# Performance work log

Measured on AMD Instinct MI355X. Metric: run time of the kernel, lower is better.

## Reference

```python
import jax, jax.numpy as jnp
import numpy as np

N = 8192
E = 262144
H = 8
D_IN = 256
D_OUT = 256
D_PRIME = D_OUT // H  # is_concat=True


def setup_inputs() -> dict:
    key = jax.random.key(0)
    k_x, k_e, k_ww, k_wb, k_aw, k_ab = jax.random.split(key, 6)
    scale_w = 1.0 / np.sqrt(D_IN)
    scale_a = 1.0 / np.sqrt(2 * D_PRIME)
    return {
        "x": jax.random.normal(k_x, (N, D_IN), dtype=jnp.float32),
        "edge_index": jax.random.randint(k_e, (2, E), 0, N, dtype=jnp.int64),
        "W_w": jax.random.uniform(k_ww, (H, D_PRIME, D_IN), jnp.float32, -scale_w, scale_w),
        "W_b": jax.random.uniform(k_wb, (H, D_PRIME), jnp.float32, -scale_w, scale_w),
        "a_w": jax.random.uniform(k_aw, (H, 1, 2 * D_PRIME), jnp.float32, -scale_a, scale_a),
        "a_b": jax.random.uniform(k_ab, (H, 1), jnp.float32, -scale_a, scale_a),
    }


def reference(x, edge_index, W_w, W_b, a_w, a_b):
    n = x.shape[0]
    vi, vj = edge_index[0], edge_index[1]
    heads = []
    for k in range(W_w.shape[0]):  # small fixed head loop
        Wx = x @ W_w[k].T + W_b[k]                       # [N, d']
        pair = jnp.concatenate([Wx[vi], Wx[vj]], axis=-1)  # [E, 2d']
        e = jax.nn.leaky_relu(pair @ a_w[k].T + a_b[k], negative_slope=0.2)[:, 0]  # [E]
        # dense NxN score matrix: non-edges keep score 0 and DO participate in softmax,
        # duplicate edges accumulate -- matches torch scatter_add_ + Softmax(dim=-1)
        A = jnp.zeros((n, n), dtype=x.dtype).at[vi, vj].add(e)
        heads.append(jax.nn.softmax(A, axis=-1) @ Wx)     # [N, d']
    xp = jnp.stack(heads)                                 # [H, N, d']
    xp = jnp.transpose(xp, (1, 0, 2)).reshape(n, -1)      # is_concat=True
    return jax.nn.elu(xp)
```

## Files before the change

kernel.cpp:

```cpp
#include <hip/hip_runtime.h>
#include <hip/hip_fp16.h>


constexpr int N_NODES = 8192;
constexpr int E_EDGES = 262144;
constexpr int DIN = 256;
constexpr int DOUT = 256;
constexpr int MAXROW = 96;
constexpr unsigned POISON = 0xAAAAAAAAu;

constexpr int BUCKET_BLOCKS = E_EDGES / (256 * 4);
constexpr int GEMM_BLOCKS = (N_NODES / 128) * 8;

typedef __attribute__((ext_vector_type(8))) short bf16x8;
typedef __attribute__((ext_vector_type(4))) float f32x4;

__device__ __forceinline__ float leaky02(float v) { return v > 0.f ? v : 0.2f * v; }

__device__ __forceinline__ float4 ldh4(const __half* p) {
    int2 r = *(const int2*)p;
    __half2 a = *(__half2*)&r.x;
    __half2 b = *(__half2*)&r.y;
    float2 fa = __half22float2(a);
    float2 fb = __half22float2(b);
    return make_float4(fa.x, fa.y, fb.x, fb.y);
}

__device__ __forceinline__ void split4(const float4 v, int2& hi, int2& lo) {
    unsigned u0 = __float_as_uint(v.x), u1 = __float_as_uint(v.y);
    unsigned u2 = __float_as_uint(v.z), u3 = __float_as_uint(v.w);
    unsigned h0 = u0 & 0xffff0000u, h1 = u1 & 0xffff0000u;
    unsigned h2 = u2 & 0xffff0000u, h3 = u3 & 0xffff0000u;
    hi.x = (int)((u0 >> 16) | h1);
    hi.y = (int)((u2 >> 16) | h3);
    float l0 = v.x - __uint_as_float(h0);
    float l1 = v.y - __uint_as_float(h1);
    float l2 = v.z - __uint_as_float(h2);
    float l3 = v.w - __uint_as_float(h3);
    lo.x = (int)((__float_as_uint(l0) >> 16) | (__float_as_uint(l1) & 0xffff0000u));
    lo.y = (int)((__float_as_uint(l2) >> 16) | (__float_as_uint(l3) & 0xffff0000u));
}

__global__ __launch_bounds__(256) void gemm_bucket(
    const float* __restrict__ x, const float* __restrict__ W,
    const float* __restrict__ Wb, const float* __restrict__ a_w,
    const int* __restrict__ eidx,
    __half* __restrict__ Wx, float* __restrict__ asrc_t,
    float* __restrict__ adst_t, float* __restrict__ colsum,
    unsigned* __restrict__ counts, int* __restrict__ colbuf)
{
    __shared__ short Whi[32][264], Wlo[32][264];
    __shared__ short Ahi[2][128][40], Alo[2][128][40];
    const int t = threadIdx.x;

    if (blockIdx.x < BUCKET_BLOCKS) {
        const int e0 = blockIdx.x * 1024 + t * 4;
        const int4 vi4 = *(const int4*)&eidx[e0];
        const int4 vj4 = *(const int4*)&eidx[E_EDGES + e0];
        unsigned c;
        c = atomicAdd(&counts[vi4.x], 1u) - POISON; if (c < MAXROW) colbuf[(size_t)vi4.x * MAXROW + c] = vj4.x;
        c = atomicAdd(&counts[vi4.y], 1u) - POISON; if (c < MAXROW) colbuf[(size_t)vi4.y * MAXROW + c] = vj4.y;
        c = atomicAdd(&counts[vi4.z], 1u) - POISON; if (c < MAXROW) colbuf[(size_t)vi4.z * MAXROW + c] = vj4.z;
        c = atomicAdd(&counts[vi4.w], 1u) - POISON; if (c < MAXROW) colbuf[(size_t)vi4.w * MAXROW + c] = vj4.w;
        return;
    }

    const int gb = blockIdx.x - BUCKET_BLOCKS;
    const int bm = gb >> 3;
    const int h  = gb & 7;
    const int r0 = bm * 128;
    const int w = t >> 6;
    const int lane = t & 63;
    const int lanen = lane & 15, quad = lane >> 4;

    float4 wl[8], al[4];
#pragma unroll
    for (int j = 0; j < 8; ++j) {
        const int idx = j * 256 + t;
        const int n = idx >> 6, q = idx & 63;
        wl[j] = *(const float4*)&W[((size_t)(h * 32 + n)) * DIN + q * 4];
    }
#pragma unroll
    for (int j = 0; j < 4; ++j) {
        const int idx = j * 256 + t;
        const int row = idx >> 3, q = idx & 7;
        al[j] = *(const float4*)&x[(size_t)(r0 + row) * DIN + q * 4];
    }
#pragma unroll
    for (int j = 0; j < 8; ++j) {
        const int idx = j * 256 + t;
        const int n = idx >> 6, q = idx & 63;
        int2 hi, lo;
        split4(wl[j], hi, lo);
        *(int2*)&Whi[n][q * 4] = hi;
        *(int2*)&Wlo[n][q * 4] = lo;
    }
#pragma unroll
    for (int j = 0; j < 4; ++j) {
        const int idx = j * 256 + t;
        const int row = idx >> 3, q = idx & 7;
        int2 hi, lo;
        split4(al[j], hi, lo);
        *(int2*)&Ahi[0][row][q * 4] = hi;
        *(int2*)&Alo[0][row][q * 4] = lo;
    }

    f32x4 acc[2][2] = {};

    for (int c = 0; c < 8; ++c) {
        __syncthreads();
        float4 nv[4];
        if (c < 7) {
#pragma unroll
            for (int j = 0; j < 4; ++j) {
                const int idx = j * 256 + t;
                const int row = idx >> 3, q = idx & 7;
                nv[j] = *(const float4*)&x[(size_t)(r0 + row) * DIN + (c + 1) * 32 + q * 4];
            }
        }
        const int buf = c & 1;
        bf16x8 bh0 = *(const bf16x8*)&Whi[lanen][c * 32 + quad * 8];
        bf16x8 bl0 = *(const bf16x8*)&Wlo[lanen][c * 32 + quad * 8];
        bf16x8 bh1 = *(const bf16x8*)&Whi[16 + lanen][c * 32 + quad * 8];
        bf16x8 bl1 = *(const bf16x8*)&Wlo[16 + lanen][c * 32 + quad * 8];
#pragma unroll
        for (int ms = 0; ms < 2; ++ms) {
            const int arow = w * 32 + ms * 16 + lanen;
            bf16x8 ah = *(const bf16x8*)&Ahi[buf][arow][quad * 8];
            bf16x8 al2 = *(const bf16x8*)&Alo[buf][arow][quad * 8];
            acc[ms][0] = __builtin_amdgcn_mfma_f32_16x16x32_bf16(ah, bh0, acc[ms][0], 0, 0, 0);
            acc[ms][0] = __builtin_amdgcn_mfma_f32_16x16x32_bf16(ah, bl0, acc[ms][0], 0, 0, 0);
            acc[ms][0] = __builtin_amdgcn_mfma_f32_16x16x32_bf16(al2, bh0, acc[ms][0], 0, 0, 0);
            acc[ms][1] = __builtin_amdgcn_mfma_f32_16x16x32_bf16(ah, bh1, acc[ms][1], 0, 0, 0);
            acc[ms][1] = __builtin_amdgcn_mfma_f32_16x16x32_bf16(ah, bl1, acc[ms][1], 0, 0, 0);
            acc[ms][1] = __builtin_amdgcn_mfma_f32_16x16x32_bf16(al2, bh1, acc[ms][1], 0, 0, 0);
        }
        if (c < 7) {
            const int nbuf = (c + 1) & 1;
#pragma unroll
            for (int j = 0; j < 4; ++j) {
                const int idx = j * 256 + t;
                const int row = idx >> 3, q = idx & 7;
                int2 hi, lo;
                split4(nv[j], hi, lo);
                *(int2*)&Ahi[nbuf][row][q * 4] = hi;
                *(int2*)&Alo[nbuf][row][q * 4] = lo;
            }
        }
    }

    const float bias0 = Wb[h * 32 + lanen];
    const float bias1 = Wb[h * 32 + 16 + lanen];
    const float aws0 = a_w[h * 64 + lanen];
    const float aws1 = a_w[h * 64 + 16 + lanen];
    const float awd0 = a_w[h * 64 + 32 + lanen];
    const float awd1 = a_w[h * 64 + 48 + lanen];
    float cs0 = 0.f, cs1 = 0.f;

#pragma unroll
    for (int ms = 0; ms < 2; ++ms) {
        const int rowb = r0 + w * 32 + ms * 16 + quad * 4;
        float ps[4], pd[4];
#pragma unroll
        for (int r = 0; r < 4; ++r) {
            const float a0 = acc[ms][0][r] + bias0;
            const float a1 = acc[ms][1][r] + bias1;
            Wx[(size_t)(rowb + r) * DOUT + h * 32 + lanen] = __float2half_rn(a0);
            Wx[(size_t)(rowb + r) * DOUT + h * 32 + 16 + lanen] = __float2half_rn(a1);
            ps[r] = a0 * aws0 + a1 * aws1;
            pd[r] = a0 * awd0 + a1 * awd1;
            cs0 += a0;
            cs1 += a1;
        }
#pragma unroll
        for (int msk = 1; msk <= 8; msk <<= 1)
#pragma unroll
            for (int r = 0; r < 4; ++r) {
                ps[r] += __shfl_xor(ps[r], msk);
                pd[r] += __shfl_xor(pd[r], msk);
            }
        if (lanen == 0) {
#pragma unroll
            for (int r = 0; r < 4; ++r) {
                asrc_t[(size_t)(rowb + r) * 8 + h] = ps[r];
                adst_t[(size_t)(rowb + r) * 8 + h] = pd[r];
            }
        }
    }
#pragma unroll
    for (int msk = 16; msk <= 32; msk <<= 1) {
        cs0 += __shfl_xor(cs0, msk);
        cs1 += __shfl_xor(cs1, msk);
    }
    if (lane < 16) {
        atomicAdd(&colsum[h * 32 + lanen], cs0);
        atomicAdd(&colsum[h * 32 + 16 + lanen], cs1);
    }
}

__global__ __launch_bounds__(256) void row_softmax(
    const unsigned* __restrict__ counts, const int* __restrict__ colbuf,
    const __half* __restrict__ Wx, const float* __restrict__ asrc_t,
    const float* __restrict__ adst_t, const float* __restrict__ a_b,
    const float* __restrict__ colsum, float* __restrict__ out)
{
    const int w = threadIdx.x >> 6;
    const int lane = threadIdx.x & 63;
    const int i = blockIdx.x * 4 + w;

    __shared__ alignas(16) int   colsL[4][MAXROW];
    __shared__ alignas(16) float wv[4][MAXROW][8];
    __shared__ alignas(16) float sv[4][MAXROW];
    __shared__ alignas(16) float base_s[4][8];

    int len = (int)(counts[i] - POISON);
    if ((unsigned)len > MAXROW) len = MAXROW;

    for (int p = lane; p < len; p += 64) colsL[w][p] = colbuf[(size_t)i * MAXROW + p];
    __builtin_amdgcn_wave_barrier();

    if (len <= 64) {
        const bool act = lane < len;
        const int c = act ? colsL[w][lane] : 0;
        const int c_cmp = act ? c : (0x40000000 + lane);
        bool dupb = false;
        for (int k = 1; k < 64; ++k) {
            int cq = __shfl(c_cmp, (lane - k) & 63);
            dupb = dupb || ((k <= lane) && (cq == c_cmp));
        }
        const bool isrep = act && !dupb;
        const int nd = __popcll(__ballot(isrep));
        const bool anydup = (nd != len);
        const float fnd = (float)(N_NODES - nd);

#pragma unroll
        for (int ck = 0; ck < 2; ++ck) {
            const float4 as = *(const float4*)&asrc_t[(size_t)i * 8 + ck * 4];
            const float4 ab = *(const float4*)&a_b[ck * 4];
            const float4 ad = *(const float4*)&adst_t[(size_t)c * 8 + ck * 4];
            float s[4], sm[4];
            s[0] = leaky02(as.x + ab.x + ad.x);
            s[1] = leaky02(as.y + ab.y + ad.y);
            s[2] = leaky02(as.z + ab.z + ad.z);
            s[3] = leaky02(as.w + ab.w + ad.w);
#pragma unroll
            for (int hh = 0; hh < 4; ++hh) sm[hh] = s[hh];

            if (anydup) {
                for (int k = 1; k < 64; ++k) {
                    const int sl = (lane + k) & 63;
                    const int cq = __shfl(c_cmp, sl);
                    float sq[4];
#pragma unroll
                    for (int hh = 0; hh < 4; ++hh) sq[hh] = __shfl(s[hh], sl);
                    if (cq == c_cmp) {
#pragma unroll
                        for (int hh = 0; hh < 4; ++hh) sm[hh] += sq[hh];
                    }
                }
            }

            float val[4];
#pragma unroll
            for (int hh = 0; hh < 4; ++hh) val[hh] = isrep ? sm[hh] : 0.f;
#pragma unroll
            for (int st = 32; st; st >>= 1)
#pragma unroll
                for (int hh = 0; hh < 4; ++hh) val[hh] = fmaxf(val[hh], __shfl_xor(val[hh], st));
            float enm[4], e[4];
#pragma unroll
            for (int hh = 0; hh < 4; ++hh) {
                float m = fmaxf(val[hh], 0.f);
                enm[hh] = __expf(-m);
                e[hh] = isrep ? __expf(sm[hh] - m) : 0.f;
                val[hh] = e[hh];
            }
#pragma unroll
            for (int st = 32; st; st >>= 1)
#pragma unroll
                for (int hh = 0; hh < 4; ++hh) val[hh] += __shfl_xor(val[hh], st);
            float wt[4];
#pragma unroll
            for (int hh = 0; hh < 4; ++hh) {
                float invZ = 1.f / (val[hh] + fnd * enm[hh]);
                wt[hh] = isrep ? (e[hh] - enm[hh]) * invZ : 0.f;
                enm[hh] *= invZ;
            }
            if (act) {
                float4 wq; wq.x = wt[0]; wq.y = wt[1]; wq.z = wt[2]; wq.w = wt[3];
                *(float4*)&wv[w][lane][ck * 4] = wq;
            }
            if (lane == 0) {
                float4 bq; bq.x = enm[0]; bq.y = enm[1]; bq.z = enm[2]; bq.w = enm[3];
                *(float4*)&base_s[w][ck * 4] = bq;
            }
        }
    } else {
        int repf0 = 0, repf1 = 0;
        {
            int p = lane;
            if (p < len) {
                int cc = colsL[w][p]; int r = 1;
                for (int q = 0; q < p; ++q) if (colsL[w][q] == cc) { r = 0; break; }
                repf0 = r;
            }
            p = lane + 64;
            if (p < len) {
                int cc = colsL[w][p]; int r = 1;
                for (int q = 0; q < p; ++q) if (colsL[w][q] == cc) { r = 0; break; }
                repf1 = r;
            }
        }
        int ndloc = repf0 + repf1;
#pragma unroll
        for (int st = 32; st; st >>= 1) ndloc += __shfl_xor(ndloc, st);
        const int nd = ndloc;
        for (int hh = 0; hh < 8; ++hh) {
            const float sabh = asrc_t[(size_t)i * 8 + hh] + a_b[hh];
            for (int p = lane; p < len; p += 64)
                sv[w][p] = leaky02(sabh + adst_t[(size_t)colsL[w][p] * 8 + hh]);
            __builtin_amdgcn_wave_barrier();
            float lmax = -1e30f, sm0 = 0.f, sm1 = 0.f;
            if (lane < len && repf0) {
                int cc = colsL[w][lane]; float a = sv[w][lane];
                for (int q = lane + 1; q < len; ++q) if (colsL[w][q] == cc) a += sv[w][q];
                sm0 = a; lmax = fmaxf(lmax, a);
            }
            if (lane + 64 < len && repf1) {
                int cc = colsL[w][lane + 64]; float a = sv[w][lane + 64];
                for (int q = lane + 65; q < len; ++q) if (colsL[w][q] == cc) a += sv[w][q];
                sm1 = a; lmax = fmaxf(lmax, a);
            }
#pragma unroll
            for (int st = 32; st; st >>= 1) lmax = fmaxf(lmax, __shfl_xor(lmax, st));
            const float mh = fmaxf(lmax, 0.f), enm = __expf(-mh);
            float e0 = (lane < len && repf0) ? __expf(sm0 - mh) : 0.f;
            float e1 = (lane + 64 < len && repf1) ? __expf(sm1 - mh) : 0.f;
            float lsum = e0 + e1;
#pragma unroll
            for (int st = 32; st; st >>= 1) lsum += __shfl_xor(lsum, st);
            const float Z = lsum + (float)(N_NODES - nd) * enm, invZ = 1.f / Z;
            if (lane == 0) base_s[w][hh] = enm * invZ;
            if (lane < len)      wv[w][lane][hh]      = repf0 ? (e0 - enm) * invZ : 0.f;
            if (lane + 64 < len) wv[w][lane + 64][hh] = repf1 ? (e1 - enm) * invZ : 0.f;
            __builtin_amdgcn_wave_barrier();
        }
    }

    const int len8 = (len + 7) & ~7;
    for (int p = len + lane; p < len8; p += 64) {
        colsL[w][p] = 0;
        float4 z; z.x = 0.f; z.y = 0.f; z.z = 0.f; z.w = 0.f;
        *(float4*)&wv[w][p][0] = z;
        *(float4*)&wv[w][p][4] = z;
    }
    __builtin_amdgcn_wave_barrier();

    const int h4 = lane >> 3;
    const float bsel = base_s[w][h4];
    const int col4 = lane * 4;

    float4 acc0; acc0.x = 0.f; acc0.y = 0.f; acc0.z = 0.f; acc0.w = 0.f;
    float4 acc1 = acc0;
    for (int p0 = 0; p0 < len8; p0 += 8) {
        const int4 ca = *(const int4*)&colsL[w][p0];
        const int4 cb = *(const int4*)&colsL[w][p0 + 4];
        const float4 v0 = ldh4(&Wx[(size_t)ca.x * DOUT + col4]);
        const float4 v1 = ldh4(&Wx[(size_t)ca.y * DOUT + col4]);
        const float4 v2 = ldh4(&Wx[(size_t)ca.z * DOUT + col4]);
        const float4 v3 = ldh4(&Wx[(size_t)ca.w * DOUT + col4]);
        const float4 v4 = ldh4(&Wx[(size_t)cb.x * DOUT + col4]);
        const float4 v5 = ldh4(&Wx[(size_t)cb.y * DOUT + col4]);
        const float4 v6 = ldh4(&Wx[(size_t)cb.z * DOUT + col4]);
        const float4 v7 = ldh4(&Wx[(size_t)cb.w * DOUT + col4]);
        const float w0 = wv[w][p0 + 0][h4];
        const float w1 = wv[w][p0 + 1][h4];
        const float w2 = wv[w][p0 + 2][h4];
        const float w3 = wv[w][p0 + 3][h4];
        const float w4 = wv[w][p0 + 4][h4];
        const float w5 = wv[w][p0 + 5][h4];
        const float w6 = wv[w][p0 + 6][h4];
        const float w7 = wv[w][p0 + 7][h4];
        acc0.x = fmaf(w0, v0.x, acc0.x); acc0.y = fmaf(w0, v0.y, acc0.y);
        acc0.z = fmaf(w0, v0.z, acc0.z); acc0.w = fmaf(w0, v0.w, acc0.w);
        acc1.x = fmaf(w1, v1.x, acc1.x); acc1.y = fmaf(w1, v1.y, acc1.y);
        acc1.z = fmaf(w1, v1.z, acc1.z); acc1.w = fmaf(w1, v1.w, acc1.w);
        acc0.x = fmaf(w2, v2.x, acc0.x); acc0.y = fmaf(w2, v2.y, acc0.y);
        acc0.z = fmaf(w2, v2.z, acc0.z); acc0.w = fmaf(w2, v2.w, acc0.w);
        acc1.x = fmaf(w3, v3.x, acc1.x); acc1.y = fmaf(w3, v3.y, acc1.y);
        acc1.z = fmaf(w3, v3.z, acc1.z); acc1.w = fmaf(w3, v3.w, acc1.w);
        acc0.x = fmaf(w4, v4.x, acc0.x); acc0.y = fmaf(w4, v4.y, acc0.y);
        acc0.z = fmaf(w4, v4.z, acc0.z); acc0.w = fmaf(w4, v4.w, acc0.w);
        acc1.x = fmaf(w5, v5.x, acc1.x); acc1.y = fmaf(w5, v5.y, acc1.y);
        acc1.z = fmaf(w5, v5.z, acc1.z); acc1.w = fmaf(w5, v5.w, acc1.w);
        acc0.x = fmaf(w6, v6.x, acc0.x); acc0.y = fmaf(w6, v6.y, acc0.y);
        acc0.z = fmaf(w6, v6.z, acc0.z); acc0.w = fmaf(w6, v6.w, acc0.w);
        acc1.x = fmaf(w7, v7.x, acc1.x); acc1.y = fmaf(w7, v7.y, acc1.y);
        acc1.z = fmaf(w7, v7.z, acc1.z); acc1.w = fmaf(w7, v7.w, acc1.w);
    }
    const float4 cs = *(const float4*)&colsum[col4];
    float4 o;
    o.x = fmaf(bsel, cs.x, acc0.x + acc1.x);
    o.y = fmaf(bsel, cs.y, acc0.y + acc1.y);
    o.z = fmaf(bsel, cs.z, acc0.z + acc1.z);
    o.w = fmaf(bsel, cs.w, acc0.w + acc1.w);
    o.x = o.x > 0.f ? o.x : expm1f(o.x);
    o.y = o.y > 0.f ? o.y : expm1f(o.y);
    o.z = o.z > 0.f ? o.z : expm1f(o.z);
    o.w = o.w > 0.f ? o.w : expm1f(o.w);
    *(float4*)&out[(size_t)i * DOUT + col4] = o;
}

extern "C" void kernel_launch(void* const* d_in, const int* in_sizes, int n_in,
                              void* d_out, int out_size, void* d_ws, size_t ws_size,
                              hipStream_t stream) {
    const float* x   = (const float*)d_in[0];
    const int*   ei  = (const int*)d_in[1];
    const float* W_w = (const float*)d_in[2];
    const float* W_b = (const float*)d_in[3];
    const float* a_w = (const float*)d_in[4];
    const float* a_b = (const float*)d_in[5];
    float* out = (float*)d_out;

    char* ws = (char*)d_ws;
    size_t off = 0;
    __half* Wx = (__half*)(ws + off);      off += (size_t)N_NODES * DOUT * 2;
    float* colsum = (float*)(ws + off);    off += DOUT * 4;
    unsigned* counts = (unsigned*)(ws + off); off += (size_t)N_NODES * 4;
    int* colbuf = (int*)(ws + off);        off += (size_t)N_NODES * MAXROW * 4;
    float* asrc_t = (float*)(ws + off);    off += (size_t)N_NODES * 8 * 4;
    float* adst_t = (float*)(ws + off);    off += (size_t)N_NODES * 8 * 4;
    (void)ws_size; (void)in_sizes; (void)n_in; (void)out_size;

    gemm_bucket<<<BUCKET_BLOCKS + GEMM_BLOCKS, 256, 0, stream>>>(
        x, W_w, W_b, a_w, ei, Wx, asrc_t, adst_t, colsum, counts, colbuf);
    row_softmax<<<N_NODES / 4, 256, 0, stream>>>(counts, colbuf, Wx, asrc_t,
                                                 adst_t, a_b, colsum, out);
}
```

Before: 132.1 us.

## Fuse GEMM, bucketing and row softmax into one cooperative grid-synced kernel

Merges the two kernels into a single cooperative launch of 512 blocks. Each block first buckets its share of edges, then computes one GEMM tile, then waits at a grid-wide sync before handling 16 rows of the softmax-aggregate phase. Shared memory is reused between the phases through a union. The aim is to drop the second launch and the gap between kernels. In exchange the grid is capped at 512 blocks, which lowers parallelism in the softmax phase, and the grid sync adds its own cost. The fused kernel also has to fit co-residency limits for the cooperative launch.

```diff
diff --git a/kernel.cpp b/kernel.cpp
--- a/kernel.cpp
+++ b/kernel.cpp
@@ -1,5 +1,8 @@
 #include <hip/hip_runtime.h>
 #include <hip/hip_fp16.h>
+#include <hip/hip_cooperative_groups.h>
+
+namespace cg = cooperative_groups;
 
 
 constexpr int N_NODES = 8192;
@@ -9,8 +12,8 @@
 constexpr int MAXROW = 96;
 constexpr unsigned POISON = 0xAAAAAAAAu;
 
-constexpr int BUCKET_BLOCKS = E_EDGES / (256 * 4);
-constexpr int GEMM_BLOCKS = (N_NODES / 128) * 8;
+constexpr int NBLK = 512;
+constexpr int EDGES_PER_BLK = E_EDGES / NBLK;
 
 typedef __attribute__((ext_vector_type(8))) short bf16x8;
 typedef __attribute__((ext_vector_type(4))) float f32x4;
@@ -41,374 +44,377 @@
     lo.y = (int)((__float_as_uint(l2) >> 16) | (__float_as_uint(l3) & 0xffff0000u));
 }
 
-__global__ __launch_bounds__(256) void gemm_bucket(
+__global__ __launch_bounds__(256) void gat_fused(
     const float* __restrict__ x, const float* __restrict__ W,
     const float* __restrict__ Wb, const float* __restrict__ a_w,
-    const int* __restrict__ eidx,
+    const int* __restrict__ eidx, const float* __restrict__ a_b,
     __half* __restrict__ Wx, float* __restrict__ asrc_t,
     float* __restrict__ adst_t, float* __restrict__ colsum,
-    unsigned* __restrict__ counts, int* __restrict__ colbuf)
+    unsigned* __restrict__ counts, int* __restrict__ colbuf,
+    float* __restrict__ out)
 {
-    __shared__ short Whi[32][264], Wlo[32][264];
-    __shared__ short Ahi[2][128][40], Alo[2][128][40];
+    __shared__ union {
+        struct {
+            short Whi[32][264], Wlo[32][264];
+            short Ahi[2][128][40], Alo[2][128][40];
+        } g;
+        struct {
+            int   colsL[4][MAXROW];
+            float wv[4][MAXROW][8];
+            float sv[4][MAXROW];
+            float base_s[4][8];
+        } s;
+    } smem;
+
     const int t = threadIdx.x;
-
-    if (blockIdx.x < BUCKET_BLOCKS) {
-        const int e0 = blockIdx.x * 1024 + t * 4;
-        const int4 vi4 = *(const int4*)&eidx[e0];
-        const int4 vj4 = *(const int4*)&eidx[E_EDGES + e0];
-        unsigned c;
-        c = atomicAdd(&counts[vi4.x], 1u) - POISON; if (c < MAXROW) colbuf[(size_t)vi4.x * MAXROW + c] = vj4.x;
-        c = atomicAdd(&counts[vi4.y], 1u) - POISON; if (c < MAXROW) colbuf[(size_t)vi4.y * MAXROW + c] = vj4.y;
-        c = atomicAdd(&counts[vi4.z], 1u) - POISON; if (c < MAXROW) colbuf[(size_t)vi4.z * MAXROW + c] = vj4.z;
-        c = atomicAdd(&counts[vi4.w], 1u) - POISON; if (c < MAXROW) colbuf[(size_t)vi4.w * MAXROW + c] = vj4.w;
-        return;
-    }
-
-    const int gb = blockIdx.x - BUCKET_BLOCKS;
-    const int bm = gb >> 3;
-    const int h  = gb & 7;
-    const int r0 = bm * 128;
     const int w = t >> 6;
     const int lane = t & 63;
-    const int lanen = lane & 15, quad = lane >> 4;
-
-    float4 wl[8], al[4];
-#pragma unroll
-    for (int j = 0; j < 8; ++j) {
-        const int idx = j * 256 + t;
-        const int n = idx >> 6, q = idx & 63;
-        wl[j] = *(const float4*)&W[((size_t)(h * 32 + n)) * DIN + q * 4];
+
+    {
+        const int e0 = blockIdx.x * EDGES_PER_BLK + t * 2;
+        const int2 vi2 = *(const int2*)&eidx[e0];
+        const int2 vj2 = *(const int2*)&eidx[E_EDGES + e0];
+        unsigned c;
+        c = atomicAdd(&counts[vi2.x], 1u) - POISON; if (c < MAXROW) colbuf[(size_t)vi2.x * MAXROW + c] = vj2.x;
+        c = atomicAdd(&counts[vi2.y], 1u) - POISON; if (c < MAXROW) colbuf[(size_t)vi2.y * MAXROW + c] = vj2.y;
     }
-#pragma unroll
-    for (int j = 0; j < 4; ++j) {
-        const int idx = j * 256 + t;
-        const int row = idx >> 3, q = idx & 7;
-        al[j] = *(const float4*)&x[(size_t)(r0 + row) * DIN + q * 4];
+
+    {
+        const int gb = blockIdx.x;
+        const int bm = gb >> 3;
+        const int h  = gb & 7;
+        const int r0 = bm * 128;
+        const int lanen = lane & 15, quad = lane >> 4;
+
+        float4 wl[8], al[4];
+#pragma unroll
+        for (int j = 0; j < 8; ++j) {
+            const int idx = j * 256 + t;
+            const int n = idx >> 6, q = idx & 63;
+            wl[j] = *(const float4*)&W[((size_t)(h * 32 + n)) * DIN + q * 4];
+        }
+#pragma unroll
+        for (int j = 0; j < 4; ++j) {
+            const int idx = j * 256 + t;
+            const int row = idx >> 3, q = idx & 7;
+            al[j] = *(const float4*)&x[(size_t)(r0 + row) * DIN + q * 4];
+        }
+#pragma unroll
+        for (int j = 0; j < 8; ++j) {
+            const int idx = j * 256 + t;
+            const int n = idx >> 6, q = idx & 63;
+            int2 hi, lo;
+            split4(wl[j], hi, lo);
+            *(int2*)&smem.g.Whi[n][q * 4] = hi;
+            *(int2*)&smem.g.Wlo[n][q * 4] = lo;
+        }
+#pragma unroll
+        for (int j = 0; j < 4; ++j) {
+            const int idx = j * 256 + t;
+            const int row = idx >> 3, q = idx & 7;
+            int2 hi, lo;
+            split4(al[j], hi, lo);
+            *(int2*)&smem.g.Ahi[0][row][q * 4] = hi;
+            *(int2*)&smem.g.Alo[0][row][q * 4] = lo;
+        }
+
+        f32x4 acc[2][2] = {};
+
+        for (int c = 0; c < 8; ++c) {
+            __syncthreads();
+            float4 nv[4];
+            if (c < 7) {
+#pragma unroll
+                for (int j = 0; j < 4; ++j) {
+                    const int idx = j * 256 + t;
+                    const int row = idx >> 3, q = idx & 7;
+                    nv[j] = *(const float4*)&x[(size_t)(r0 + row) * DIN + (c + 1) * 32 + q * 4];
+                }
+            }
+            const int buf = c & 1;
+            bf16x8 bh0 = *(const bf16x8*)&smem.g.Whi[lanen][c * 32 + quad * 8];
+            bf16x8 bl0 = *(const bf16x8*)&smem.g.Wlo[lanen][c * 32 + quad * 8];
+            bf16x8 bh1 = *(const bf16x8*)&smem.g.Whi[16 + lanen][c * 32 + quad * 8];
+            bf16x8 bl1 = *(const bf16x8*)&smem.g.Wlo[16 + lanen][c * 32 + quad * 8];
+#pragma unroll
+            for (int ms = 0; ms < 2; ++ms) {
+                const int arow = w * 32 + ms * 16 + lanen;
+                bf16x8 ah = *(const bf16x8*)&smem.g.Ahi[buf][arow][quad * 8];
+                bf16x8 al2 = *(const bf16x8*)&smem.g.Alo[buf][arow][quad * 8];
+                acc[ms][0] = __builtin_amdgcn_mfma_f32_16x16x32_bf16(ah, bh0, acc[ms][0], 0, 0, 0);
+                acc[ms][0] = __builtin_amdgcn_mfma_f32_16x16x32_bf16(ah, bl0, acc[ms][0], 0, 0, 0);
+                acc[ms][0] = __builtin_amdgcn_mfma_f32_16x16x32_bf16(al2, bh0, acc[ms][0], 0, 0, 0);
+                acc[ms][1] = __builtin_amdgcn_mfma_f32_16x16x32_bf16(ah, bh1, acc[ms][1], 0, 0, 0);
+                acc[ms][1] = __builtin_amdgcn_mfma_f32_16x16x32_bf16(ah, bl1, acc[ms][1], 0, 0, 0);
+                acc[ms][1] = __builtin_amdgcn_mfma_f32_16x16x32_bf16(al2, bh1, acc[ms][1], 0, 0, 0);
+            }
+            if (c < 7) {
+                const int nbuf = (c + 1) & 1;
+#pragma unroll
+                for (int j = 0; j < 4; ++j) {
+                    const int idx = j * 256 + t;
+                    const int row = idx >> 3, q = idx & 7;
+                    int2 hi, lo;
+                    split4(nv[j], hi, lo);
+                    *(int2*)&smem.g.Ahi[nbuf][row][q * 4] = hi;
+                    *(int2*)&smem.g.Alo[nbuf][row][q * 4] = lo;
+                }
+            }
+        }
+
+        const float bias0 = Wb[h * 32 + lanen];
+        const float bias1 = Wb[h * 32 + 16 + lanen];
+        const float aws0 = a_w[h * 64 + lanen];
+        const float aws1 = a_w[h * 64 + 16 + lanen];
+        const float awd0 = a_w[h * 64 + 32 + lanen];
+        const float awd1 = a_w[h * 64 + 48 + lanen];
+        float cs0 = 0.f, cs1 = 0.f;
+
+#pragma unroll
+        for (int ms = 0; ms < 2; ++ms) {
+            const int rowb = r0 + w * 32 + ms * 16 + quad * 4;
+            float ps[4], pd[4];
+#pragma unroll
+            for (int r = 0; r < 4; ++r) {
+                const float a0 = acc[ms][0][r] + bias0;
+                const float a1 = acc[ms][1][r] + bias1;
+                Wx[(size_t)(rowb + r) * DOUT + h * 32 + lanen] = __float2half_rn(a0);
+                Wx[(size_t)(rowb + r) * DOUT + h * 32 + 16 + lanen] = __float2half_rn(a1);
+                ps[r] = a0 * aws0 + a1 * aws1;
+                pd[r] = a0 * awd0 + a1 * awd1;
+                cs0 += a0;
+                cs1 += a1;
+            }
+#pragma unroll
+            for (int msk = 1; msk <= 8; msk <<= 1)
+#pragma unroll
+                for (int r = 0; r < 4; ++r) {
+                    ps[r] += __shfl_xor(ps[r], msk);
+                    pd[r] += __shfl_xor(pd[r], msk);
+                }
+            if (lanen == 0) {
+#pragma unroll
+                for (int r = 0; r < 4; ++r) {
+                    asrc_t[(size_t)(rowb + r) * 8 + h] = ps[r];
+                    adst_t[(size_t)(rowb + r) * 8 + h] = pd[r];
+                }
+            }
+        }
+#pragma unroll
+        for (int msk = 16; msk <= 32; msk <<= 1) {
+            cs0 += __shfl_xor(cs0, msk);
+            cs1 += __shfl_xor(cs1, msk);
+        }
+        if (lane < 16) {
+            atomicAdd(&colsum[h * 32 + lanen], cs0);
+            atomicAdd(&colsum[h * 32 + 16 + lanen], cs1);
+        }
     }
-#pragma unroll
-    for (int j = 0; j < 8; ++j) {
-        const int idx = j * 256 + t;
-        const int n = idx >> 6, q = idx & 63;
-        int2 hi, lo;
-        split4(wl[j], hi, lo);
-        *(int2*)&Whi[n][q * 4] = hi;
-        *(int2*)&Wlo[n][q * 4] = lo;
+
+    cg::this_grid().sync();
+
+    for (int rr = 0; rr < 4; ++rr) {
+        const int i = blockIdx.x * 16 + w * 4 + rr;
+
+        int len = (int)(counts[i] - POISON);
+        if ((unsigned)len > MAXROW) len = MAXROW;
+
+        for (int p = lane; p < len; p += 64) smem.s.colsL[w][p] = colbuf[(size_t)i * MAXROW + p];
+        __builtin_amdgcn_wave_barrier();
+
+        if (len <= 64) {
+            const bool act = lane < len;
+            const int c = act ? smem.s.colsL[w][lane] : 0;
+            const int c_cmp = act ? c : (0x40000000 + lane);
+            bool dupb = false;
+            for (int k = 1; k < 64; ++k) {
+                int cq = __shfl(c_cmp, (lane - k) & 63);
+                dupb = dupb || ((k <= lane) && (cq == c_cmp));
+            }
+            const bool isrep = act && !dupb;
+            const int nd = __popcll(__ballot(isrep));
+            const bool anydup = (nd != len);
+            const float fnd = (float)(N_NODES - nd);
+
+#pragma unroll
+            for (int ck = 0; ck < 2; ++ck) {
+                const float4 as = *(const float4*)&asrc_t[(size_t)i * 8 + ck * 4];
+                const float4 ab = *(const float4*)&a_b[ck * 4];
+                const float4 ad = *(const float4*)&adst_t[(size_t)c * 8 + ck * 4];
+                float s[4], sm[4];
+                s[0] = leaky02(as.x + ab.x + ad.x);
+                s[1] = leaky02(as.y + ab.y + ad.y);
+                s[2] = leaky02(as.z + ab.z + ad.z);
+                s[3] = leaky02(as.w + ab.w + ad.w);
+#pragma unroll
+                for (int hh = 0; hh < 4; ++hh) sm[hh] = s[hh];
+
+                if (anydup) {
+                    for (int k = 1; k < 64; ++k) {
+                        const int sl = (lane + k) & 63;
+                        const int cq = __shfl(c_cmp, sl);
+                        float sq[4];
+#pragma unroll
+                        for (int hh = 0; hh < 4; ++hh) sq[hh] = __shfl(s[hh], sl);
+                        if (cq == c_cmp) {
+#pragma unroll
+                            for (int hh = 0; hh < 4; ++hh) sm[hh] += sq[hh];
+                        }
+                    }
+                }
+
+                float val[4];
+#pragma unroll
+                for (int hh = 0; hh < 4; ++hh) val[hh] = isrep ? sm[hh] : 0.f;
+#pragma unroll
+                for (int st = 32; st; st >>= 1)
+#pragma unroll
+                    for (int hh = 0; hh < 4; ++hh) val[hh] = fmaxf(val[hh], __shfl_xor(val[hh], st));
+                float enm[4], e[4];
+#pragma unroll
+                for (int hh = 0; hh < 4; ++hh) {
+                    float m = fmaxf(val[hh], 0.f);
+                    enm[hh] = __expf(-m);
+                    e[hh] = isrep ? __expf(sm[hh] - m) : 0.f;
+                    val[hh] = e[hh];
+                }
+#pragma unroll
+                for (int st = 32; st; st >>= 1)
+#pragma unroll
+                    for (int hh = 0; hh < 4; ++hh) val[hh] += __shfl_xor(val[hh], st);
+                float wt[4];
+#pragma unroll
+                for (int hh = 0; hh < 4; ++hh) {
+                    float invZ = 1.f / (val[hh] + fnd * enm[hh]);
+                    wt[hh] = isrep ? (e[hh] - enm[hh]) * invZ : 0.f;
+                    enm[hh] *= invZ;
+                }
+                if (act) {
+                    float4 wq; wq.x = wt[0]; wq.y = wt[1]; wq.z = wt[2]; wq.w = wt[3];
+                    *(float4*)&smem.s.wv[w][lane][ck * 4] = wq;
+                }
+                if (lane == 0) {
+                    float4 bq; bq.x = enm[0]; bq.y = enm[1]; bq.z = enm[2]; bq.w = enm[3];
+                    *(float4*)&smem.s.base_s[w][ck * 4] = bq;
+                }
+            }
+        } else {
+            int repf0 = 0, repf1 = 0;
+            {
+                int p = lane;
+                if (p < len) {
+                    int cc = smem.s.colsL[w][p]; int r = 1;
+                    for (int q = 0; q < p; ++q) if (smem.s.colsL[w][q] == cc) { r = 0; break; }
+                    repf0 = r;
+                }
+                p = lane + 64;
+                if (p < len) {
+                    int cc = smem.s.colsL[w][p]; int r = 1;
+                    for (int q = 0; q < p; ++q) if (smem.s.colsL[w][q] == cc) { r = 0; break; }
+                    repf1 = r;
+                }
+            }
+            int ndloc = repf0 + repf1;
+#pragma unroll
+            for (int st = 32; st; st >>= 1) ndloc += __shfl_xor(ndloc, st);
+            const int nd = ndloc;
+            for (int hh = 0; hh < 8; ++hh) {
+                const float sabh = asrc_t[(size_t)i * 8 + hh] + a_b[hh];
+                for (int p = lane; p < len; p += 64)
+                    smem.s.sv[w][p] = leaky02(sabh + adst_t[(size_t)smem.s.colsL[w][p] * 8 + hh]);
+                __builtin_amdgcn_wave_barrier();
+                float lmax = -1e30f, sm0 = 0.f, sm1 = 0.f;
+                if (lane < len && repf0) {
+                    int cc = smem.s.colsL[w][lane]; float a = smem.s.sv[w][lane];
+                    for (int q = lane + 1; q < len; ++q) if (smem.s.colsL[w][q] == cc) a += smem.s.sv[w][q];
+                    sm0 = a; lmax = fmaxf(lmax, a);
+                }
+                if (lane + 64 < len && repf1) {
+                    int cc = smem.s.colsL[w][lane + 64]; float a = smem.s.sv[w][lane + 64];
+                    for (int q = lane + 65; q < len; ++q) if (smem.s.colsL[w][q] == cc) a += smem.s.sv[w][q];
+                    sm1 = a; lmax = fmaxf(lmax, a);
+                }
+#pragma unroll
+                for (int st = 32; st; st >>= 1) lmax = fmaxf(lmax, __shfl_xor(lmax, st));
+                const float mh = fmaxf(lmax, 0.f), enm = __expf(-mh);
+                float e0 = (lane < len && repf0) ? __expf(sm0 - mh) : 0.f;
+                float e1 = (lane + 64 < len && repf1) ? __expf(sm1 - mh) : 0.f;
+                float lsum = e0 + e1;
+#pragma unroll
+                for (int st = 32; st; st >>= 1) lsum += __shfl_xor(lsum, st);
+                const float Z = lsum + (float)(N_NODES - nd) * enm, invZ = 1.f / Z;
+                if (lane == 0) smem.s.base_s[w][hh] = enm * invZ;
+                if (lane < len)      smem.s.wv[w][lane][hh]      = repf0 ? (e0 - enm) * invZ : 0.f;
+                if (lane + 64 < len) smem.s.wv[w][lane + 64][hh] = repf1 ? (e1 - enm) * invZ : 0.f;
+                __builtin_amdgcn_wave_barrier();
+            }
+        }
+
+        const int len8 = (len + 7) & ~7;
+        for (int p = len + lane; p < len8; p += 64) {
+            smem.s.colsL[w][p] = 0;
+            float4 z; z.x = 0.f; z.y = 0.f; z.z = 0.f; z.w = 0.f;
+            *(float4*)&smem.s.wv[w][p][0] = z;
+            *(float4*)&smem.s.wv[w][p][4] = z;
+        }
+        __builtin_amdgcn_wave_barrier();
+
+        const int h4 = lane >> 3;
+        const float bsel = smem.s.base_s[w][h4];
+        const int col4 = lane * 4;
+
+        float4 acc0; acc0.x = 0.f; acc0.y = 0.f; acc0.z = 0.f; acc0.w = 0.f;
+        float4 acc1 = acc0;
+        for (int p0 = 0; p0 < len8; p0 += 8) {
+            const int4 ca = *(const int4*)&smem.s.colsL[w][p0];
+            const int4 cb = *(const int4*)&smem.s.colsL[w][p0 + 4];
+            const float4 v0 = ldh4(&Wx[(size_t)ca.x * DOUT + col4]);
+            const float4 v1 = ldh4(&Wx[(size_t)ca.y * DOUT + col4]);
+            const float4 v2 = ldh4(&Wx[(size_t)ca.z * DOUT + col4]);
+            const float4 v3 = ldh4(&Wx[(size_t)ca.w * DOUT + col4]);
+            const float4 v4 = ldh4(&Wx[(size_t)cb.x * DOUT + col4]);
+            const float4 v5 = ldh4(&Wx[(size_t)cb.y * DOUT + col4]);
+            const float4 v6 = ldh4(&Wx[(size_t)cb.z * DOUT + col4]);
+            const float4 v7 = ldh4(&Wx[(size_t)cb.w * DOUT + col4]);
+            const float w0 = smem.s.wv[w][p0 + 0][h4];
+            const float w1 = smem.s.wv[w][p0 + 1][h4];
+            const float w2 = smem.s.wv[w][p0 + 2][h4];
+            const float w3 = smem.s.wv[w][p0 + 3][h4];
+            const float w4 = smem.s.wv[w][p0 + 4][h4];
+            const float w5 = smem.s.wv[w][p0 + 5][h4];
+            const float w6 = smem.s.wv[w][p0 + 6][h4];
+            const float w7 = smem.s.wv[w][p0 + 7][h4];
+            acc0.x = fmaf(w0, v0.x, acc0.x); acc0.y = fmaf(w0, v0.y, acc0.y);
+            acc0.z = fmaf(w0, v0.z, acc0.z); acc0.w = fmaf(w0, v0.w, acc0.w);
+            acc1.x = fmaf(w1, v1.x, acc1.x); acc1.y = fmaf(w1, v1.y, acc1.y);
+            acc1.z = fmaf(w1, v1.z, acc1.z); acc1.w = fmaf(w1, v1.w, acc1.w);
+            acc0.x = fmaf(w2, v2.x, acc0.x); acc0.y = fmaf(w2, v2.y, acc0.y);
+            acc0.z = fmaf(w2, v2.z, acc0.z); acc0.w = fmaf(w2, v2.w, acc0.w);
+            acc1.x = fmaf(w3, v3.x, acc1.x); acc1.y = fmaf(w3, v3.y, acc1.y);
+            acc1.z = fmaf(w3, v3.z, acc1.z); acc1.w = fmaf(w3, v3.w, acc1.w);
+            acc0.x = fmaf(w4, v4.x, acc0.x); acc0.y = fmaf(w4, v4.y, acc0.y);
+            acc0.z = fmaf(w4, v4.z, acc0.z); acc0.w = fmaf(w4, v4.w, acc0.w);
+            acc1.x = fmaf(w5, v5.x, acc1.x); acc1.y = fmaf(w5, v5.y, acc1.y);
+            acc1.z = fmaf(w5, v5.z, acc1.z); acc1.w = fmaf(w5, v5.w, acc1.w);
+            acc0.x = fmaf(w6, v6.x, acc0.x); acc0.y = fmaf(w6, v6.y, acc0.y);
+            acc0.z = fmaf(w6, v6.z, acc0.z); acc0.w = fmaf(w6, v6.w, acc0.w);
+            acc1.x = fmaf(w7, v7.x, acc1.x); acc1.y = fmaf(w7, v7.y, acc1.y);
+            acc1.z = fmaf(w7, v7.z, acc1.z); acc1.w = fmaf(w7, v7.w, acc1.w);
+        }
+        const float4 cs = *(const float4*)&colsum[col4];
+        float4 o;
+        o.x = fmaf(bsel, cs.x, acc0.x + acc1.x);
+        o.y = fmaf(bsel, cs.y, acc0.y + acc1.y);
+        o.z = fmaf(bsel, cs.z, acc0.z + acc1.z);
+        o.w = fmaf(bsel, cs.w, acc0.w + acc1.w);
+        o.x = o.x > 0.f ? o.x : expm1f(o.x);
+        o.y = o.y > 0.f ? o.y : expm1f(o.y);
+        o.z = o.z > 0.f ? o.z : expm1f(o.z);
+        o.w = o.w > 0.f ? o.w : expm1f(o.w);
+        *(float4*)&out[(size_t)i * DOUT + col4] = o;
+
+        __builtin_amdgcn_wave_barrier();
     }
-#pragma unroll
-    for (int j = 0; j < 4; ++j) {
-        const int idx = j * 256 + t;
-        const int row = idx >> 3, q = idx & 7;
-        int2 hi, lo;
-        split4(al[j], hi, lo);
-        *(int2*)&Ahi[0][row][q * 4] = hi;
-        *(int2*)&Alo[0][row][q * 4] = lo;
-    }
-
-    f32x4 acc[2][2] = {};
-
-    for (int c = 0; c < 8; ++c) {
-        __syncthreads();
-        float4 nv[4];
-        if (c < 7) {
-#pragma unroll
-            for (int j = 0; j < 4; ++j) {
-                const int idx = j * 256 + t;
-                const int row = idx >> 3, q = idx & 7;
-                nv[j] = *(const float4*)&x[(size_t)(r0 + row) * DIN + (c + 1) * 32 + q * 4];
-            }
-        }
-        const int buf = c & 1;
-        bf16x8 bh0 = *(const bf16x8*)&Whi[lanen][c * 32 + quad * 8];
-        bf16x8 bl0 = *(const bf16x8*)&Wlo[lanen][c * 32 + quad * 8];
-        bf16x8 bh1 = *(const bf16x8*)&Whi[16 + lanen][c * 32 + quad * 8];
-        bf16x8 bl1 = *(const bf16x8*)&Wlo[16 + lanen][c * 32 + quad * 8];
-#pragma unroll
-        for (int ms = 0; ms < 2; ++ms) {
-            const int arow = w * 32 + ms * 16 + lanen;
-            bf16x8 ah = *(const bf16x8*)&Ahi[buf][arow][quad * 8];
-            bf16x8 al2 = *(const bf16x8*)&Alo[buf][arow][quad * 8];
-            acc[ms][0] = __builtin_amdgcn_mfma_f32_16x16x32_bf16(ah, bh0, acc[ms][0], 0, 0, 0);
-            acc[ms][0] = __builtin_amdgcn_mfma_f32_16x16x32_bf16(ah, bl0, acc[ms][0], 0, 0, 0);
-            acc[ms][0] = __builtin_amdgcn_mfma_f32_16x16x32_bf16(al2, bh0, acc[ms][0], 0, 0, 0);
-            acc[ms][1] = __builtin_amdgcn_mfma_f32_16x16x32_bf16(ah, bh1, acc[ms][1], 0, 0, 0);
-            acc[ms][1] = __builtin_amdgcn_mfma_f32_16x16x32_bf16(ah, bl1, acc[ms][1], 0, 0, 0);
-            acc[ms][1] = __builtin_amdgcn_mfma_f32_16x16x32_bf16(al2, bh1, acc[ms][1], 0, 0, 0);
-        }
-        if (c < 7) {
-            const int nbuf = (c + 1) & 1;
-#pragma unroll
-            for (int j = 0; j < 4; ++j) {
-                const int idx = j * 256 + t;
-                const int row = idx >> 3, q = idx & 7;
-                int2 hi, lo;
-                split4(nv[j], hi, lo);
-                *(int2*)&Ahi[nbuf][row][q * 4] = hi;
-                *(int2*)&Alo[nbuf][row][q * 4] = lo;
-            }
-        }
-    }
-
-    const float bias0 = Wb[h * 32 + lanen];
-    const float bias1 = Wb[h * 32 + 16 + lanen];
-    const float aws0 = a_w[h * 64 + lanen];
-    const float aws1 = a_w[h * 64 + 16 + lanen];
-    const float awd0 = a_w[h * 64 + 32 + lanen];
-    const float awd1 = a_w[h * 64 + 48 + lanen];
-    float cs0 = 0.f, cs1 = 0.f;
-
-#pragma unroll
-    for (int ms = 0; ms < 2; ++ms) {
-        const int rowb = r0 + w * 32 + ms * 16 + quad * 4;
-        float ps[4], pd[4];
-#pragma unroll
-        for (int r = 0; r < 4; ++r) {
-            const float a0 = acc[ms][0][r] + bias0;
-            const float a1 = acc[ms][1][r] + bias1;
-            Wx[(size_t)(rowb + r) * DOUT + h * 32 + lanen] = __float2half_rn(a0);
-            Wx[(size_t)(rowb + r) * DOUT + h * 32 + 16 + lanen] = __float2half_rn(a1);
-            ps[r] = a0 * aws0 + a1 * aws1;
-            pd[r] = a0 * awd0 + a1 * awd1;
-            cs0 += a0;
-            cs1 += a1;
-        }
-#pragma unroll
-        for (int msk = 1; msk <= 8; msk <<= 1)
-#pragma unroll
-            for (int r = 0; r < 4; ++r) {
-                ps[r] += __shfl_xor(ps[r], msk);
-                pd[r] += __shfl_xor(pd[r], msk);
-            }
-        if (lanen == 0) {
-#pragma unroll
-            for (int r = 0; r < 4; ++r) {
-                asrc_t[(size_t)(rowb + r) * 8 + h] = ps[r];
-                adst_t[(size_t)(rowb + r) * 8 + h] = pd[r];
-            }
-        }
-    }
-#pragma unroll
-    for (int msk = 16; msk <= 32; msk <<= 1) {
-        cs0 += __shfl_xor(cs0, msk);
-        cs1 += __shfl_xor(cs1, msk);
-    }
-    if (lane < 16) {
-        atomicAdd(&colsum[h * 32 + lanen], cs0);
-        atomicAdd(&colsum[h * 32 + 16 + lanen], cs1);
-    }
-}
-
-__global__ __launch_bounds__(256) void row_softmax(
-    const unsigned* __restrict__ counts, const int* __restrict__ colbuf,
-    const __half* __restrict__ Wx, const float* __restrict__ asrc_t,
-    const float* __restrict__ adst_t, const float* __restrict__ a_b,
-    const float* __restrict__ colsum, float* __restrict__ out)
-{
-    const int w = threadIdx.x >> 6;
-    const int lane = threadIdx.x & 63;
-    const int i = blockIdx.x * 4 + w;
-
-    __shared__ alignas(16) int   colsL[4][MAXROW];
-    __shared__ alignas(16) float wv[4][MAXROW][8];
-    __shared__ alignas(16) float sv[4][MAXROW];
-    __shared__ alignas(16) float base_s[4][8];
-
-    int len = (int)(counts[i] - POISON);
-    if ((unsigned)len > MAXROW) len = MAXROW;
-
-    for (int p = lane; p < len; p += 64) colsL[w][p] = colbuf[(size_t)i * MAXROW + p];
-    __builtin_amdgcn_wave_barrier();
-
-    if (len <= 64) {
-        const bool act = lane < len;
-        const int c = act ? colsL[w][lane] : 0;
-        const int c_cmp = act ? c : (0x40000000 + lane);
-        bool dupb = false;
-        for (int k = 1; k < 64; ++k) {
-            int cq = __shfl(c_cmp, (lane - k) & 63);
-            dupb = dupb || ((k <= lane) && (cq == c_cmp));
-        }
-        const bool isrep = act && !dupb;
-        const int nd = __popcll(__ballot(isrep));
-        const bool anydup = (nd != len);
-        const float fnd = (float)(N_NODES - nd);
-
-#pragma unroll
-        for (int ck = 0; ck < 2; ++ck) {
-            const float4 as = *(const float4*)&asrc_t[(size_t)i * 8 + ck * 4];
-            const float4 ab = *(const float4*)&a_b[ck * 4];
-            const float4 ad = *(const float4*)&adst_t[(size_t)c * 8 + ck * 4];
-            float s[4], sm[4];
-            s[0] = leaky02(as.x + ab.x + ad.x);
-            s[1] = leaky02(as.y + ab.y + ad.y);
-            s[2] = leaky02(as.z + ab.z + ad.z);
-            s[3] = leaky02(as.w + ab.w + ad.w);
-#pragma unroll
-            for (int hh = 0; hh < 4; ++hh) sm[hh] = s[hh];
-
-            if (anydup) {
-                for (int k = 1; k < 64; ++k) {
-                    const int sl = (lane + k) & 63;
-                    const int cq = __shfl(c_cmp, sl);
-                    float sq[4];
-#pragma unroll
-                    for (int hh = 0; hh < 4; ++hh) sq[hh] = __shfl(s[hh], sl);
-                    if (cq == c_cmp) {
-#pragma unroll
-                        for (int hh = 0; hh < 4; ++hh) sm[hh] += sq[hh];
-                    }
-                }
-            }
-
-            float val[4];
-#pragma unroll
-            for (int hh = 0; hh < 4; ++hh) val[hh] = isrep ? sm[hh] : 0.f;
-#pragma unroll
-            for (int st = 32; st; st >>= 1)
-#pragma unroll
-                for (int hh = 0; hh < 4; ++hh) val[hh] = fmaxf(val[hh], __shfl_xor(val[hh], st));
-            float enm[4], e[4];
-#pragma unroll
-            for (int hh = 0; hh < 4; ++hh) {
-                float m = fmaxf(val[hh], 0.f);
-                enm[hh] = __expf(-m);
-                e[hh] = isrep ? __expf(sm[hh] - m) : 0.f;
-                val[hh] = e[hh];
-            }
-#pragma unroll
-            for (int st = 32; st; st >>= 1)
-#pragma unroll
-                for (int hh = 0; hh < 4; ++hh) val[hh] += __shfl_xor(val[hh], st);
-            float wt[4];
-#pragma unroll
-            for (int hh = 0; hh < 4; ++hh) {
-                float invZ = 1.f / (val[hh] + fnd * enm[hh]);
-                wt[hh] = isrep ? (e[hh] - enm[hh]) * invZ : 0.f;
-                enm[hh] *= invZ;
-            }
-            if (act) {
-                float4 wq; wq.x = wt[0]; wq.y = wt[1]; wq.z = wt[2]; wq.w = wt[3];
-                *(float4*)&wv[w][lane][ck * 4] = wq;
-            }
-            if (lane == 0) {
-                float4 bq; bq.x = enm[0]; bq.y = enm[1]; bq.z = enm[2]; bq.w = enm[3];
-                *(float4*)&base_s[w][ck * 4] = bq;
-            }
-        }
-    } else {
-        int repf0 = 0, repf1 = 0;
-        {
-            int p = lane;
-            if (p < len) {
-                int cc = colsL[w][p]; int r = 1;
-                for (int q = 0; q < p; ++q) if (colsL[w][q] == cc) { r = 0; break; }
-                repf0 = r;
-            }
-            p = lane + 64;
-            if (p < len) {
-                int cc = colsL[w][p]; int r = 1;
-                for (int q = 0; q < p; ++q) if (colsL[w][q] == cc) { r = 0; break; }
-                repf1 = r;
-            }
-        }
-        int ndloc = repf0 + repf1;
-#pragma unroll
-        for (int st = 32; st; st >>= 1) ndloc += __shfl_xor(ndloc, st);
-        const int nd = ndloc;
-        for (int hh = 0; hh < 8; ++hh) {
-            const float sabh = asrc_t[(size_t)i * 8 + hh] + a_b[hh];
-            for (int p = lane; p < len; p += 64)
-                sv[w][p] = leaky02(sabh + adst_t[(size_t)colsL[w][p] * 8 + hh]);
-            __builtin_amdgcn_wave_barrier();
-            float lmax = -1e30f, sm0 = 0.f, sm1 = 0.f;
-            if (lane < len && repf0) {
-                int cc = colsL[w][lane]; float a = sv[w][lane];
-                for (int q = lane + 1; q < len; ++q) if (colsL[w][q] == cc) a += sv[w][q];
-                sm0 = a; lmax = fmaxf(lmax, a);
-            }
-            if (lane + 64 < len && repf1) {
-                int cc = colsL[w][lane + 64]; float a = sv[w][lane + 64];
-                for (int q = lane + 65; q < len; ++q) if (colsL[w][q] == cc) a += sv[w][q];
-                sm1 = a; lmax = fmaxf(lmax, a);
-            }
-#pragma unroll
-            for (int st = 32; st; st >>= 1) lmax = fmaxf(lmax, __shfl_xor(lmax, st));
-            const float mh = fmaxf(lmax, 0.f), enm = __expf(-mh);
-            float e0 = (lane < len && repf0) ? __expf(sm0 - mh) : 0.f;
-            float e1 = (lane + 64 < len && repf1) ? __expf(sm1 - mh) : 0.f;
-            float lsum = e0 + e1;
-#pragma unroll
-            for (int st = 32; st; st >>= 1) lsum += __shfl_xor(lsum, st);
-            const float Z = lsum + (float)(N_NODES - nd) * enm, invZ = 1.f / Z;
-            if (lane == 0) base_s[w][hh] = enm * invZ;
-            if (lane < len)      wv[w][lane][hh]      = repf0 ? (e0 - enm) * invZ : 0.f;
-            if (lane + 64 < len) wv[w][lane + 64][hh] = repf1 ? (e1 - enm) * invZ : 0.f;
-            __builtin_amdgcn_wave_barrier();
-        }
-    }
-
-    const int len8 = (len + 7) & ~7;
-    for (int p = len + lane; p < len8; p += 64) {
-        colsL[w][p] = 0;
-        float4 z; z.x = 0.f; z.y = 0.f; z.z = 0.f; z.w = 0.f;
-        *(float4*)&wv[w][p][0] = z;
-        *(float4*)&wv[w][p][4] = z;
-    }
-    __builtin_amdgcn_wave_barrier();
-
-    const int h4 = lane >> 3;
-    const float bsel = base_s[w][h4];
-    const int col4 = lane * 4;
-
-    float4 acc0; acc0.x = 0.f; acc0.y = 0.f; acc0.z = 0.f; acc0.w = 0.f;
-    float4 acc1 = acc0;
-    for (int p0 = 0; p0 < len8; p0 += 8) {
-        const int4 ca = *(const int4*)&colsL[w][p0];
-        const int4 cb = *(const int4*)&colsL[w][p0 + 4];
-        const float4 v0 = ldh4(&Wx[(size_t)ca.x * DOUT + col4]);
-        const float4 v1 = ldh4(&Wx[(size_t)ca.y * DOUT + col4]);
-        const float4 v2 = ldh4(&Wx[(size_t)ca.z * DOUT + col4]);
-        const float4 v3 = ldh4(&Wx[(size_t)ca.w * DOUT + col4]);
-        const float4 v4 = ldh4(&Wx[(size_t)cb.x * DOUT + col4]);
-        const float4 v5 = ldh4(&Wx[(size_t)cb.y * DOUT + col4]);
-        const float4 v6 = ldh4(&Wx[(size_t)cb.z * DOUT + col4]);
-        const float4 v7 = ldh4(&Wx[(size_t)cb.w * DOUT + col4]);
-        const float w0 = wv[w][p0 + 0][h4];
-        const float w1 = wv[w][p0 + 1][h4];
-        const float w2 = wv[w][p0 + 2][h4];
-        const float w3 = wv[w][p0 + 3][h4];
-        const float w4 = wv[w][p0 + 4][h4];
-        const float w5 = wv[w][p0 + 5][h4];
-        const float w6 = wv[w][p0 + 6][h4];
-        const float w7 = wv[w][p0 + 7][h4];
-        acc0.x = fmaf(w0, v0.x, acc0.x); acc0.y = fmaf(w0, v0.y, acc0.y);
-        acc0.z = fmaf(w0, v0.z, acc0.z); acc0.w = fmaf(w0, v0.w, acc0.w);
-        acc1.x = fmaf(w1, v1.x, acc1.x); acc1.y = fmaf(w1, v1.y, acc1.y);
-        acc1.z = fmaf(w1, v1.z, acc1.z); acc1.w = fmaf(w1, v1.w, acc1.w);
-        acc0.x = fmaf(w2, v2.x, acc0.x); acc0.y = fmaf(w2, v2.y, acc0.y);
-        acc0.z = fmaf(w2, v2.z, acc0.z); acc0.w = fmaf(w2, v2.w, acc0.w);
-        acc1.x = fmaf(w3, v3.x, acc1.x); acc1.y = fmaf(w3, v3.y, acc1.y);
-        acc1.z = fmaf(w3, v3.z, acc1.z); acc1.w = fmaf(w3, v3.w, acc1.w);
-        acc0.x = fmaf(w4, v4.x, acc0.x); acc0.y = fmaf(w4, v4.y, acc0.y);
-        acc0.z = fmaf(w4, v4.z, acc0.z); acc0.w = fmaf(w4, v4.w, acc0.w);
-        acc1.x = fmaf(w5, v5.x, acc1.x); acc1.y = fmaf(w5, v5.y, acc1.y);
-        acc1.z = fmaf(w5, v5.z, acc1.z); acc1.w = fmaf(w5, v5.w, acc1.w);
-        acc0.x = fmaf(w6, v6.x, acc0.x); acc0.y = fmaf(w6, v6.y, acc0.y);
-        acc0.z = fmaf(w6, v6.z, acc0.z); acc0.w = fmaf(w6, v6.w, acc0.w);
-        acc1.x = fmaf(w7, v7.x, acc1.x); acc1.y = fmaf(w7, v7.y, acc1.y);
-        acc1.z = fmaf(w7, v7.z, acc1.z); acc1.w = fmaf(w7, v7.w, acc1.w);
-    }
-    const float4 cs = *(const float4*)&colsum[col4];
-    float4 o;
-    o.x = fmaf(bsel, cs.x, acc0.x + acc1.x);
-    o.y = fmaf(bsel, cs.y, acc0.y + acc1.y);
-    o.z = fmaf(bsel, cs.z, acc0.z + acc1.z);
-    o.w = fmaf(bsel, cs.w, acc0.w + acc1.w);
-    o.x = o.x > 0.f ? o.x : expm1f(o.x);
-    o.y = o.y > 0.f ? o.y : expm1f(o.y);
-    o.z = o.z > 0.f ? o.z : expm1f(o.z);
-    o.w = o.w > 0.f ? o.w : expm1f(o.w);
-    *(float4*)&out[(size_t)i * DOUT + col4] = o;
 }
 
 extern "C" void kernel_launch(void* const* d_in, const int* in_sizes, int n_in,
@@ -432,8 +438,11 @@
     float* adst_t = (float*)(ws + off);    off += (size_t)N_NODES * 8 * 4;
     (void)ws_size; (void)in_sizes; (void)n_in; (void)out_size;
 
-    gemm_bucket<<<BUCKET_BLOCKS + GEMM_BLOCKS, 256, 0, stream>>>(
-        x, W_w, W_b, a_w, ei, Wx, asrc_t, adst_t, colsum, counts, colbuf);
-    row_softmax<<<N_NODES / 4, 256, 0, stream>>>(counts, colbuf, Wx, asrc_t,
-                                                 adst_t, a_b, colsum, out);
+    void* args[] = {
+        (void*)&x, (void*)&W_w, (void*)&W_b, (void*)&a_w, (void*)&ei, (void*)&a_b,
+        (void*)&Wx, (void*)&asrc_t, (void*)&adst_t, (void*)&colsum,
+        (void*)&counts, (void*)&colbuf, (void*)&out
+    };
+    hipLaunchCooperativeKernel((const void*)gat_fused, dim3(NBLK), dim3(256),
+                               args, 0, stream);
 }
```

Result: slower. 216.7 us (+64.1%).
